# Kernel tuning notes

Hardware: AMD Instinct MI355X
Metric: run time of the kernel (lower is better)

## Reference

```python
import jax, jax.numpy as jnp
import numpy as np

DIM = 256
NUM_HEADS = 4
HEAD_DIM = DIM // NUM_HEADS


def setup_inputs() -> dict:
    key = jax.random.key(0)
    ks = jax.random.split(key, 8)
    B, N, C = 4, 2048, DIM
    x = jax.random.normal(ks[0], (B, N, C), dtype=jnp.float32)
    R = jax.random.normal(ks[1], (B, 3, 3), dtype=jnp.float32)
    P = jax.random.normal(ks[2], (N, 3), dtype=jnp.float32)
    s = 1.0 / np.sqrt(C)
    qkv_w = jax.random.normal(ks[3], (3 * C, C), dtype=jnp.float32) * s
    qkv_b = jax.random.normal(ks[4], (3 * C,), dtype=jnp.float32) * 0.02
    proj_w = jax.random.normal(ks[5], (C, C), dtype=jnp.float32) * s
    proj_b = jax.random.normal(ks[6], (C,), dtype=jnp.float32) * 0.02
    pos_scale = jnp.asarray(1.0, dtype=jnp.float32)
    return {"x": x, "R": R, "P": P, "qkv_w": qkv_w, "qkv_b": qkv_b,
            "proj_w": proj_w, "proj_b": proj_b, "pos_scale": pos_scale}


def reference(x, R, P, qkv_w, qkv_b, proj_w, proj_b, pos_scale):
    B, N, C = x.shape
    H, D = NUM_HEADS, HEAD_DIM
    scale = D ** -0.5
    # qkv: (B,N,3C) -> (3,B,H,N,D)
    qkv = (x @ qkv_w.T + qkv_b).reshape(B, N, 3, H, D).transpose(2, 0, 3, 1, 4)
    q, k, v = qkv[0], qkv[1], qkv[2]
    # attention logits (B,H,N,N)
    attn = jnp.einsum('bhid,bhjd->bhij', q, k) * scale
    # positional bias: RP = (R @ P^T)^T -> (B,N,3); bias_ij = dot(RP_i, P_j)
    RP = jnp.einsum('bab,jb->bja', R, P) if False else jnp.einsum('bca,ja->bjc', jnp.swapaxes(R, 1, 2), P)
    RP = jnp.einsum('bcd,jd->bjc', R, P)  # (B,N,3): (R @ P.T).T
    bias = jnp.einsum('bik,jk->bij', RP, P)[:, None, :, :] * pos_scale  # (B,1,N,N) broadcast over heads
    attn = jax.nn.softmax(attn + bias, axis=-1)
    out = jnp.einsum('bhij,bhjd->bhid', attn, v)  # (B,H,N,D)
    out = out.transpose(0, 2, 1, 3).reshape(B, N, C)
    out = out @ proj_w.T + proj_b
    return out
```

## Files before the change

kernel.cpp:

```cpp
#include <hip/hip_runtime.h>
#include <hip/hip_bf16.h>

#define B_ 4
#define N_ 2048
#define C_ 256
#define H_ 4
#define D_ 64

typedef __attribute__((ext_vector_type(8))) short bf16x8;
typedef __attribute__((ext_vector_type(4))) float f32x4;

#define LOG2E 1.4426950408889634f

static __device__ inline unsigned short f2bf(float f) {
    unsigned u = __builtin_bit_cast(unsigned, f);
    unsigned r = (u + 0x7fffu + ((u >> 16) & 1u)) >> 16;
    return (unsigned short)r;
}
static __device__ inline float bf2f(unsigned short h) {
    unsigned u = ((unsigned)h) << 16;
    return __builtin_bit_cast(float, u);
}
static __device__ inline unsigned pack2(float a, float b) {
    __hip_bfloat162 h = __float22bfloat162_rn(make_float2(a, b));
    unsigned u;
    __builtin_memcpy(&u, &h, 4);
    return u;
}
static __device__ inline bf16x8 ld_frag(const unsigned short* p) {
    return __builtin_bit_cast(bf16x8, *(const uint4*)p);
}

__global__ __launch_bounds__(256) void cvt_kernel(
    const float* __restrict__ x, const float* __restrict__ qkv_w,
    const float* __restrict__ proj_w,
    unsigned short* __restrict__ xb, unsigned short* __restrict__ wqb,
    unsigned short* __restrict__ wpb)
{
    const int bid = blockIdx.x, tid = threadIdx.x;
    const float* s; unsigned short* d; int i;
    if (bid < 1024)      { s = x;      d = xb;  i = (bid * 256 + tid) * 8; }
    else if (bid < 1120) { s = qkv_w;  d = wqb; i = ((bid - 1024) * 256 + tid) * 8; }
    else                 { s = proj_w; d = wpb; i = ((bid - 1120) * 256 + tid) * 8; }
    float4 a = *(const float4*)(s + i);
    float4 b = *(const float4*)(s + i + 4);
    uint4 u;
    u.x = pack2(a.x, a.y); u.y = pack2(a.z, a.w);
    u.z = pack2(b.x, b.y); u.w = pack2(b.z, b.w);
    *(uint4*)(d + i) = u;
}

__global__ __launch_bounds__(256) void qkv_gemm(
    const unsigned short* __restrict__ xb, const unsigned short* __restrict__ wb,
    const float* __restrict__ bias, unsigned short* __restrict__ qb,
    unsigned short* __restrict__ kb, unsigned short* __restrict__ vt)
{
    __shared__ __align__(16) unsigned short As[128 * 40];
    __shared__ __align__(16) unsigned short Bs[128 * 40];
    const int m0 = blockIdx.x * 128, o0 = blockIdx.y * 128;
    const int tid = threadIdx.x;
    const int wave = tid >> 6, lane = tid & 63, quad = lane >> 4, l16 = lane & 15;
    const int wy = wave >> 1, wx = wave & 1;

    f32x4 acc[4][4];
    #pragma unroll
    for (int i = 0; i < 4; ++i)
        #pragma unroll
        for (int j = 0; j < 4; ++j) acc[i][j] = (f32x4){0.f, 0.f, 0.f, 0.f};

    const int srow = tid >> 1, soff = (tid & 1) * 16;

    for (int k0 = 0; k0 < 256; k0 += 32) {
        __syncthreads();
        {
            const unsigned short* sa = &xb[(size_t)(m0 + srow) * 256 + k0 + soff];
            const unsigned short* sb = &wb[(size_t)(o0 + srow) * 256 + k0 + soff];
            *(uint4*)&As[srow * 40 + soff + 0] = *(const uint4*)(sa + 0);
            *(uint4*)&As[srow * 40 + soff + 8] = *(const uint4*)(sa + 8);
            *(uint4*)&Bs[srow * 40 + soff + 0] = *(const uint4*)(sb + 0);
            *(uint4*)&Bs[srow * 40 + soff + 8] = *(const uint4*)(sb + 8);
        }
        __syncthreads();
        bf16x8 a[4], b[4];
        #pragma unroll
        for (int mt = 0; mt < 4; ++mt) a[mt] = ld_frag(&As[(wy * 64 + mt * 16 + l16) * 40 + quad * 8]);
        #pragma unroll
        for (int nt = 0; nt < 4; ++nt) b[nt] = ld_frag(&Bs[(wx * 64 + nt * 16 + l16) * 40 + quad * 8]);
        #pragma unroll
        for (int mt = 0; mt < 4; ++mt)
            #pragma unroll
            for (int nt = 0; nt < 4; ++nt)
                acc[mt][nt] = __builtin_amdgcn_mfma_f32_16x16x32_bf16(a[mt], b[nt], acc[mt][nt], 0, 0, 0);
    }

    const int sec = o0 + wx * 64;
    const int three = sec >> 8;
    const int h = (sec >> 6) & 3;
    const int b = m0 >> 11;
    float bv[4];
    #pragma unroll
    for (int nt = 0; nt < 4; ++nt) bv[nt] = bias[sec + nt * 16 + l16];

    if (three == 2) {
        const int n64 = (m0 + wy * 64) & 2047;
        const size_t bh64 = ((size_t)b * H_ + h) * 64;
        #pragma unroll
        for (int nt = 0; nt < 4; ++nt) {
            int d = nt * 16 + l16;
            #pragma unroll
            for (int r = 0; r < 4; ++r) {
                ushort4 v;
                v.x = f2bf(acc[0][nt][r] + bv[nt]);
                v.y = f2bf(acc[1][nt][r] + bv[nt]);
                v.z = f2bf(acc[2][nt][r] + bv[nt]);
                v.w = f2bf(acc[3][nt][r] + bv[nt]);
                *(ushort4*)&vt[(bh64 + d) * N_ + n64 + 16 * quad + 4 * r] = v;
            }
        }
    } else {
        unsigned short* dst = (three == 0) ? qb : kb;
        float sc = (three == 0) ? (0.125f * LOG2E) : 1.0f;
        #pragma unroll
        for (int mt = 0; mt < 4; ++mt)
            #pragma unroll
            for (int r = 0; r < 4; ++r) {
                int n = (m0 + wy * 64 + mt * 16 + quad * 4 + r) & 2047;
                size_t rowbase = (((size_t)b * H_ + h) * N_ + n) * D_;
                #pragma unroll
                for (int nt = 0; nt < 4; ++nt)
                    dst[rowbase + nt * 16 + l16] = f2bf((acc[mt][nt][r] + bv[nt]) * sc);
            }
    }
}

#define LDK 72
#define LDKX 104

__global__ __launch_bounds__(256) void attn_kernel(
    const unsigned short* __restrict__ qb, const unsigned short* __restrict__ kb,
    const unsigned short* __restrict__ vt,
    const float* __restrict__ Rm, const float* __restrict__ Pm,
    const float* __restrict__ ps_ptr,
    unsigned short* __restrict__ Opart, float* __restrict__ ml)
{
    __shared__ __align__(16) unsigned short Ks[64 * LDKX];
    __shared__ __align__(16) unsigned short Vs[64 * LDK];
    __shared__ __align__(16) unsigned short Ps[64 * LDK];

    const int bh = blockIdx.y;
    const int b = bh >> 2;
    const int i0 = blockIdx.x * 64;
    const int split = blockIdx.z;
    const int tid = threadIdx.x;
    const int wave = tid >> 6, lane = tid & 63;
    const int quad = lane >> 4, l16 = lane & 15;
    const float ps = ps_ptr[0];

    const size_t base = (size_t)bh * N_ * D_;
    const unsigned short* qg = qb + base;
    const unsigned short* kg = kb + base;
    const unsigned short* vg = vt + base;

    if (tid < 64) {
        uint4 z = {0u, 0u, 0u, 0u};
        *(uint4*)&Ks[tid * LDKX + 80] = z;
        *(uint4*)&Ks[tid * LDKX + 88] = z;
    }

    const int qrow = i0 + wave * 16 + l16;
    bf16x8 aq[3];
    #pragma unroll
    for (int ks = 0; ks < 2; ++ks)
        aq[ks] = ld_frag(&qg[(size_t)qrow * D_ + ks * 32 + quad * 8]);

    {
        float p0 = Pm[qrow * 3 + 0], p1 = Pm[qrow * 3 + 1], p2 = Pm[qrow * 3 + 2];
        float sc = ps * LOG2E;
        unsigned short ah[3], al[3];
        #pragma unroll
        for (int c = 0; c < 3; ++c) {
            float a = (Rm[b * 9 + c * 3 + 0] * p0 + Rm[b * 9 + c * 3 + 1] * p1
                     + Rm[b * 9 + c * 3 + 2] * p2) * sc;
            ah[c] = f2bf(a);
            al[c] = f2bf(a - bf2f(ah[c]));
        }
        bf16x8 e = (bf16x8){0,0,0,0,0,0,0,0};
        if (quad == 0) {
            e[0] = (short)ah[0]; e[1] = (short)ah[1]; e[2] = (short)ah[2];
            e[3] = (short)ah[0]; e[4] = (short)ah[1]; e[5] = (short)ah[2];
            e[6] = (short)al[0]; e[7] = (short)al[1];
        } else if (quad == 1) {
            e[0] = (short)al[2];
        }
        aq[2] = e;
    }

    const bf16x8 ones = (bf16x8){0x3F80,0x3F80,0x3F80,0x3F80,0x3F80,0x3F80,0x3F80,0x3F80};

    float m_run = -1e30f;
    f32x4 o_acc[4], lacc;
    #pragma unroll
    for (int t = 0; t < 4; ++t) o_acc[t] = (f32x4){0.f, 0.f, 0.f, 0.f};
    lacc = (f32x4){0.f, 0.f, 0.f, 0.f};

    const int jbeg = split * (N_ / 2);
    const int NT = (N_ / 2) / 64;

    for (int jt = 0; jt < NT; ++jt) {
        const int j0 = jbeg + jt * 64;
        __syncthreads();
        #pragma unroll
        for (int rr = 0; rr < 2; ++rr) {
            int c = tid + rr * 256;
            int row = c >> 3, off = (c & 7) * 8;
            *(uint4*)&Ks[row * LDKX + off] = *(const uint4*)&kg[(size_t)(j0 + row) * D_ + off];
            *(uint4*)&Vs[row * LDK + off] = *(const uint4*)&vg[(size_t)row * N_ + j0 + off];
        }
        if (tid < 64) {
            const float* pp = &Pm[(size_t)(j0 + tid) * 3];
            float p0 = pp[0], p1 = pp[1], p2 = pp[2];
            unsigned u0 = f2bf(p0), u1 = f2bf(p1), u2 = f2bf(p2);
            unsigned v0 = f2bf(p0 - bf2f((unsigned short)u0));
            unsigned v1 = f2bf(p1 - bf2f((unsigned short)u1));
            unsigned v2 = f2bf(p2 - bf2f((unsigned short)u2));
            uint4 lo, hi;
            lo.x = u0 | (u1 << 16); lo.y = u2 | (v0 << 16);
            lo.z = v1 | (v2 << 16); lo.w = u0 | (u1 << 16);
            hi.x = u2; hi.y = 0u; hi.z = 0u; hi.w = 0u;
            *(uint4*)&Ks[tid * LDKX + 64] = lo;
            *(uint4*)&Ks[tid * LDKX + 72] = hi;
        }
        __syncthreads();

        f32x4 s[4];
        #pragma unroll
        for (int t = 0; t < 4; ++t) {
            f32x4 c = {0.f, 0.f, 0.f, 0.f};
            #pragma unroll
            for (int ks = 0; ks < 3; ++ks) {
                bf16x8 bk = ld_frag(&Ks[(l16 + 16 * t) * LDKX + ks * 32 + quad * 8]);
                c = __builtin_amdgcn_mfma_f32_16x16x32_bf16(aq[ks], bk, c, 0, 0, 0);
            }
            s[t] = c;
        }

        float mx = m_run;
        #pragma unroll
        for (int t = 0; t < 4; ++t)
            #pragma unroll
            for (int r = 0; r < 4; ++r)
                mx = fmaxf(mx, s[t][r]);
        #pragma unroll
        for (int off = 1; off < 64; off <<= 1)
            mx = fmaxf(mx, __shfl_xor(mx, off));
        const float alpha = exp2f(m_run - mx);
        m_run = mx;

        #pragma unroll
        for (int r = 0; r < 4; ++r) {
            float p0 = exp2f(s[0][r] - mx), p1 = exp2f(s[1][r] - mx);
            float p2 = exp2f(s[2][r] - mx), p3 = exp2f(s[3][r] - mx);
            uint2 w;
            w.x = pack2(p0, p1);
            w.y = pack2(p2, p3);
            *(uint2*)&Ps[(wave * 16 + quad * 4 + r) * LDK + 4 * l16] = w;
        }

        if (alpha < 1.0f) {
            #pragma unroll
            for (int t = 0; t < 4; ++t)
                #pragma unroll
                for (int r = 0; r < 4; ++r)
                    o_acc[t][r] *= alpha;
            #pragma unroll
            for (int r = 0; r < 4; ++r) lacc[r] *= alpha;
        }

        #pragma unroll
        for (int ks = 0; ks < 2; ++ks) {
            bf16x8 ap = ld_frag(&Ps[(wave * 16 + l16) * LDK + ks * 32 + quad * 8]);
            #pragma unroll
            for (int t = 0; t < 4; ++t) {
                bf16x8 bv = ld_frag(&Vs[(l16 + 16 * t) * LDK + ks * 32 + quad * 8]);
                o_acc[t] = __builtin_amdgcn_mfma_f32_16x16x32_bf16(ap, bv, o_acc[t], 0, 0, 0);
            }
            lacc = __builtin_amdgcn_mfma_f32_16x16x32_bf16(ap, ones, lacc, 0, 0, 0);
        }
    }

    const size_t pbase = (size_t)(split * 16 + bh) * N_;
    #pragma unroll
    for (int r = 0; r < 4; ++r) {
        int row = i0 + wave * 16 + quad * 4 + r;
        #pragma unroll
        for (int t = 0; t < 4; ++t)
            Opart[(pbase + row) * D_ + l16 + 16 * t] = f2bf(o_acc[t][r]);
        if (l16 == 0) {
            float2* mlp = (float2*)ml;
            mlp[pbase + row] = make_float2(m_run, lacc[r]);
        }
    }
}

__global__ __launch_bounds__(256) void proj_gemm(
    const unsigned short* __restrict__ Opart, const float* __restrict__ ml,
    const unsigned short* __restrict__ wb, const float* __restrict__ bias,
    float* __restrict__ out)
{
    __shared__ __align__(16) unsigned short As[64 * 40];
    __shared__ __align__(16) unsigned short Bs[64 * 40];
    const int m0 = blockIdx.x * 64, o0 = blockIdx.y * 64;
    const int tid = threadIdx.x;
    const int wave = tid >> 6, lane = tid & 63, quad = lane >> 4, l16 = lane & 15;
    const float2* mlp = (const float2*)ml;

    const int srow = tid >> 2, scb = (tid & 3) * 8;
    const int sm = m0 + srow, sb = sm >> 11, sn = sm & 2047;

    float w1h[4], w2h[4];
    #pragma unroll
    for (int h = 0; h < 4; ++h) {
        size_t r1 = (size_t)(sb * 4 + h) * N_ + sn;
        float2 ml1 = mlp[r1], ml2 = mlp[r1 + 16 * N_];
        float mm = fmaxf(ml1.x, ml2.x);
        float w1 = exp2f(ml1.x - mm), w2 = exp2f(ml2.x - mm);
        float inv = 1.f / (ml1.y * w1 + ml2.y * w2);
        w1h[h] = w1 * inv; w2h[h] = w2 * inv;
    }

    f32x4 acc[4];
    #pragma unroll
    for (int j = 0; j < 4; ++j) acc[j] = (f32x4){0.f, 0.f, 0.f, 0.f};

    for (int k0 = 0; k0 < 256; k0 += 32) {
        const int h = k0 >> 6;
        const int d0 = (k0 & 63) + scb;
        __syncthreads();
        {
            size_t r1 = (size_t)(sb * 4 + h) * N_ + sn;
            union { uint4 u; unsigned short s[8]; } a1, a2;
            a1.u = *(const uint4*)&Opart[r1 * D_ + d0];
            a2.u = *(const uint4*)&Opart[(r1 + 16 * N_) * D_ + d0];
            float w1 = w1h[h], w2 = w2h[h];
            uint4 mv;
            unsigned* mp = (unsigned*)&mv;
            #pragma unroll
            for (int j = 0; j < 4; ++j)
                mp[j] = pack2(bf2f(a1.s[2*j]) * w1 + bf2f(a2.s[2*j]) * w2,
                              bf2f(a1.s[2*j+1]) * w1 + bf2f(a2.s[2*j+1]) * w2);
            *(uint4*)&As[srow * 40 + scb] = mv;
            *(uint4*)&Bs[srow * 40 + scb] = *(const uint4*)&wb[(size_t)(o0 + srow) * 256 + k0 + scb];
        }
        __syncthreads();
        bf16x8 a = ld_frag(&As[(wave * 16 + l16) * 40 + quad * 8]);
        #pragma unroll
        for (int nt = 0; nt < 4; ++nt) {
            bf16x8 b = ld_frag(&Bs[(nt * 16 + l16) * 40 + quad * 8]);
            acc[nt] = __builtin_amdgcn_mfma_f32_16x16x32_bf16(a, b, acc[nt], 0, 0, 0);
        }
    }

    float bv[4];
    #pragma unroll
    for (int nt = 0; nt < 4; ++nt) bv[nt] = bias[o0 + nt * 16 + l16];
    #pragma unroll
    for (int r = 0; r < 4; ++r) {
        int m = m0 + wave * 16 + quad * 4 + r;
        #pragma unroll
        for (int nt = 0; nt < 4; ++nt)
            out[(size_t)m * 256 + o0 + nt * 16 + l16] = acc[nt][r] + bv[nt];
    }
}

extern "C" void kernel_launch(void* const* d_in, const int* in_sizes, int n_in,
                              void* d_out, int out_size, void* d_ws, size_t ws_size,
                              hipStream_t stream) {
    const float* x       = (const float*)d_in[0];
    const float* Rm      = (const float*)d_in[1];
    const float* Pm      = (const float*)d_in[2];
    const float* qkv_w   = (const float*)d_in[3];
    const float* qkv_b   = (const float*)d_in[4];
    const float* proj_w  = (const float*)d_in[5];
    const float* proj_b  = (const float*)d_in[6];
    const float* pos_scl = (const float*)d_in[7];
    float* out = (float*)d_out;

    const size_t NE = (size_t)B_ * H_ * N_ * D_;
    unsigned short* xb    = (unsigned short*)d_ws;
    unsigned short* wqb   = xb   + NE;
    unsigned short* wpb   = wqb  + 768 * 256;
    unsigned short* qb    = wpb  + 256 * 256;
    unsigned short* kb    = qb   + NE;
    unsigned short* vtb   = kb   + NE;
    unsigned short* opart = vtb  + NE;
    float*          mlb   = (float*)(opart + 2 * NE);

    cvt_kernel<<<1152, 256, 0, stream>>>(x, qkv_w, proj_w, xb, wqb, wpb);
    qkv_gemm<<<dim3(64, 6), 256, 0, stream>>>(xb, wqb, qkv_b, qb, kb, vtb);
    attn_kernel<<<dim3(32, 16, 2), 256, 0, stream>>>(qb, kb, vtb, Rm, Pm, pos_scl, opart, mlb);
    proj_gemm<<<dim3(128, 4), 256, 0, stream>>>(opart, mlb, wpb, proj_b, out);
}
```

Before: 140.1 us.

## Fuse all stages into one persistent kernel with grid-wide atomic barriers

```diff
diff --git a/kernel.cpp b/kernel.cpp
--- a/kernel.cpp
+++ b/kernel.cpp
@@ -6,6 +6,7 @@
 #define C_ 256
 #define H_ 4
 #define D_ 64
+#define GRID_ 512
 
 typedef __attribute__((ext_vector_type(8))) short bf16x8;
 typedef __attribute__((ext_vector_type(4))) float f32x4;
@@ -31,344 +32,320 @@
     return __builtin_bit_cast(bf16x8, *(const uint4*)p);
 }
 
-__global__ __launch_bounds__(256) void cvt_kernel(
-    const float* __restrict__ x, const float* __restrict__ qkv_w,
-    const float* __restrict__ proj_w,
-    unsigned short* __restrict__ xb, unsigned short* __restrict__ wqb,
-    unsigned short* __restrict__ wpb)
-{
-    const int bid = blockIdx.x, tid = threadIdx.x;
-    const float* s; unsigned short* d; int i;
-    if (bid < 1024)      { s = x;      d = xb;  i = (bid * 256 + tid) * 8; }
-    else if (bid < 1120) { s = qkv_w;  d = wqb; i = ((bid - 1024) * 256 + tid) * 8; }
-    else                 { s = proj_w; d = wpb; i = ((bid - 1120) * 256 + tid) * 8; }
-    float4 a = *(const float4*)(s + i);
-    float4 b = *(const float4*)(s + i + 4);
-    uint4 u;
-    u.x = pack2(a.x, a.y); u.y = pack2(a.z, a.w);
-    u.z = pack2(b.x, b.y); u.w = pack2(b.z, b.w);
-    *(uint4*)(d + i) = u;
-}
-
-__global__ __launch_bounds__(256) void qkv_gemm(
-    const unsigned short* __restrict__ xb, const unsigned short* __restrict__ wb,
-    const float* __restrict__ bias, unsigned short* __restrict__ qb,
-    unsigned short* __restrict__ kb, unsigned short* __restrict__ vt)
-{
-    __shared__ __align__(16) unsigned short As[128 * 40];
-    __shared__ __align__(16) unsigned short Bs[128 * 40];
-    const int m0 = blockIdx.x * 128, o0 = blockIdx.y * 128;
-    const int tid = threadIdx.x;
-    const int wave = tid >> 6, lane = tid & 63, quad = lane >> 4, l16 = lane & 15;
-    const int wy = wave >> 1, wx = wave & 1;
-
-    f32x4 acc[4][4];
-    #pragma unroll
-    for (int i = 0; i < 4; ++i)
-        #pragma unroll
-        for (int j = 0; j < 4; ++j) acc[i][j] = (f32x4){0.f, 0.f, 0.f, 0.f};
-
-    const int srow = tid >> 1, soff = (tid & 1) * 16;
-
-    for (int k0 = 0; k0 < 256; k0 += 32) {
-        __syncthreads();
-        {
-            const unsigned short* sa = &xb[(size_t)(m0 + srow) * 256 + k0 + soff];
-            const unsigned short* sb = &wb[(size_t)(o0 + srow) * 256 + k0 + soff];
-            *(uint4*)&As[srow * 40 + soff + 0] = *(const uint4*)(sa + 0);
-            *(uint4*)&As[srow * 40 + soff + 8] = *(const uint4*)(sa + 8);
-            *(uint4*)&Bs[srow * 40 + soff + 0] = *(const uint4*)(sb + 0);
-            *(uint4*)&Bs[srow * 40 + soff + 8] = *(const uint4*)(sb + 8);
-        }
-        __syncthreads();
-        bf16x8 a[4], b[4];
-        #pragma unroll
-        for (int mt = 0; mt < 4; ++mt) a[mt] = ld_frag(&As[(wy * 64 + mt * 16 + l16) * 40 + quad * 8]);
-        #pragma unroll
-        for (int nt = 0; nt < 4; ++nt) b[nt] = ld_frag(&Bs[(wx * 64 + nt * 16 + l16) * 40 + quad * 8]);
-        #pragma unroll
-        for (int mt = 0; mt < 4; ++mt)
-            #pragma unroll
-            for (int nt = 0; nt < 4; ++nt)
-                acc[mt][nt] = __builtin_amdgcn_mfma_f32_16x16x32_bf16(a[mt], b[nt], acc[mt][nt], 0, 0, 0);
-    }
-
-    const int sec = o0 + wx * 64;
-    const int three = sec >> 8;
-    const int h = (sec >> 6) & 3;
-    const int b = m0 >> 11;
-    float bv[4];
-    #pragma unroll
-    for (int nt = 0; nt < 4; ++nt) bv[nt] = bias[sec + nt * 16 + l16];
-
-    if (three == 2) {
-        const int n64 = (m0 + wy * 64) & 2047;
-        const size_t bh64 = ((size_t)b * H_ + h) * 64;
-        #pragma unroll
-        for (int nt = 0; nt < 4; ++nt) {
-            int d = nt * 16 + l16;
-            #pragma unroll
-            for (int r = 0; r < 4; ++r) {
-                ushort4 v;
-                v.x = f2bf(acc[0][nt][r] + bv[nt]);
-                v.y = f2bf(acc[1][nt][r] + bv[nt]);
-                v.z = f2bf(acc[2][nt][r] + bv[nt]);
-                v.w = f2bf(acc[3][nt][r] + bv[nt]);
-                *(ushort4*)&vt[(bh64 + d) * N_ + n64 + 16 * quad + 4 * r] = v;
-            }
-        }
-    } else {
-        unsigned short* dst = (three == 0) ? qb : kb;
-        float sc = (three == 0) ? (0.125f * LOG2E) : 1.0f;
-        #pragma unroll
-        for (int mt = 0; mt < 4; ++mt)
-            #pragma unroll
-            for (int r = 0; r < 4; ++r) {
-                int n = (m0 + wy * 64 + mt * 16 + quad * 4 + r) & 2047;
-                size_t rowbase = (((size_t)b * H_ + h) * N_ + n) * D_;
-                #pragma unroll
-                for (int nt = 0; nt < 4; ++nt)
-                    dst[rowbase + nt * 16 + l16] = f2bf((acc[mt][nt][r] + bv[nt]) * sc);
-            }
-    }
+static __device__ inline void gbar(unsigned* cnt, unsigned target) {
+    __syncthreads();
+    if (threadIdx.x == 0) {
+        __threadfence();
+        atomicAdd(cnt, 1u);
+        while (atomicAdd(cnt, 0u) < target)
+            __builtin_amdgcn_s_sleep(8);
+        __threadfence();
+    }
+    __syncthreads();
+}
+
+__global__ void init_kernel(unsigned* cnt) {
+    if (threadIdx.x < 4) cnt[threadIdx.x] = 0u;
 }
 
 #define LDK 72
 #define LDKX 104
 
-__global__ __launch_bounds__(256) void attn_kernel(
-    const unsigned short* __restrict__ qb, const unsigned short* __restrict__ kb,
-    const unsigned short* __restrict__ vt,
-    const float* __restrict__ Rm, const float* __restrict__ Pm,
-    const float* __restrict__ ps_ptr,
-    unsigned short* __restrict__ Opart, float* __restrict__ ml)
+__global__ __launch_bounds__(256) void fused_kernel(
+    const float* __restrict__ x, const float* __restrict__ Rm,
+    const float* __restrict__ Pm, const float* __restrict__ qkv_w,
+    const float* __restrict__ qkv_b, const float* __restrict__ proj_w,
+    const float* __restrict__ proj_b, const float* __restrict__ ps_ptr,
+    float* __restrict__ out,
+    unsigned short* __restrict__ xb, unsigned short* __restrict__ wqb,
+    unsigned short* __restrict__ wpb, unsigned short* __restrict__ qb,
+    unsigned short* __restrict__ kb, unsigned short* __restrict__ vt,
+    unsigned short* __restrict__ obuf, unsigned* __restrict__ cnt)
 {
-    __shared__ __align__(16) unsigned short Ks[64 * LDKX];
-    __shared__ __align__(16) unsigned short Vs[64 * LDK];
-    __shared__ __align__(16) unsigned short Ps[64 * LDK];
-
-    const int bh = blockIdx.y;
-    const int b = bh >> 2;
-    const int i0 = blockIdx.x * 64;
-    const int split = blockIdx.z;
+    __shared__ __align__(16) unsigned short smem[15872];
+
+    const int bid = blockIdx.x;
     const int tid = threadIdx.x;
     const int wave = tid >> 6, lane = tid & 63;
     const int quad = lane >> 4, l16 = lane & 15;
-    const float ps = ps_ptr[0];
-
-    const size_t base = (size_t)bh * N_ * D_;
-    const unsigned short* qg = qb + base;
-    const unsigned short* kg = kb + base;
-    const unsigned short* vg = vt + base;
-
-    if (tid < 64) {
-        uint4 z = {0u, 0u, 0u, 0u};
-        *(uint4*)&Ks[tid * LDKX + 80] = z;
-        *(uint4*)&Ks[tid * LDKX + 88] = z;
-    }
-
-    const int qrow = i0 + wave * 16 + l16;
-    bf16x8 aq[3];
-    #pragma unroll
-    for (int ks = 0; ks < 2; ++ks)
-        aq[ks] = ld_frag(&qg[(size_t)qrow * D_ + ks * 32 + quad * 8]);
 
     {
-        float p0 = Pm[qrow * 3 + 0], p1 = Pm[qrow * 3 + 1], p2 = Pm[qrow * 3 + 2];
-        float sc = ps * LOG2E;
-        unsigned short ah[3], al[3];
-        #pragma unroll
-        for (int c = 0; c < 3; ++c) {
-            float a = (Rm[b * 9 + c * 3 + 0] * p0 + Rm[b * 9 + c * 3 + 1] * p1
-                     + Rm[b * 9 + c * 3 + 2] * p2) * sc;
-            ah[c] = f2bf(a);
-            al[c] = f2bf(a - bf2f(ah[c]));
-        }
-        bf16x8 e = (bf16x8){0,0,0,0,0,0,0,0};
-        if (quad == 0) {
-            e[0] = (short)ah[0]; e[1] = (short)ah[1]; e[2] = (short)ah[2];
-            e[3] = (short)ah[0]; e[4] = (short)ah[1]; e[5] = (short)ah[2];
-            e[6] = (short)al[0]; e[7] = (short)al[1];
-        } else if (quad == 1) {
-            e[0] = (short)al[2];
-        }
-        aq[2] = e;
-    }
-
-    const bf16x8 ones = (bf16x8){0x3F80,0x3F80,0x3F80,0x3F80,0x3F80,0x3F80,0x3F80,0x3F80};
-
-    float m_run = -1e30f;
-    f32x4 o_acc[4], lacc;
-    #pragma unroll
-    for (int t = 0; t < 4; ++t) o_acc[t] = (f32x4){0.f, 0.f, 0.f, 0.f};
-    lacc = (f32x4){0.f, 0.f, 0.f, 0.f};
-
-    const int jbeg = split * (N_ / 2);
-    const int NT = (N_ / 2) / 64;
-
-    for (int jt = 0; jt < NT; ++jt) {
-        const int j0 = jbeg + jt * 64;
-        __syncthreads();
-        #pragma unroll
-        for (int rr = 0; rr < 2; ++rr) {
-            int c = tid + rr * 256;
-            int row = c >> 3, off = (c & 7) * 8;
-            *(uint4*)&Ks[row * LDKX + off] = *(const uint4*)&kg[(size_t)(j0 + row) * D_ + off];
-            *(uint4*)&Vs[row * LDK + off] = *(const uint4*)&vg[(size_t)row * N_ + j0 + off];
-        }
+        const int total8 = (2097152 + 196608 + 65536) / 8;
+        for (int i = bid * 256 + tid; i < total8; i += GRID_ * 256) {
+            int e = i * 8;
+            const float* s; unsigned short* d; int off;
+            if (e < 2097152)      { s = x;      d = xb;  off = e; }
+            else if (e < 2293760) { s = qkv_w;  d = wqb; off = e - 2097152; }
+            else                  { s = proj_w; d = wpb; off = e - 2293760; }
+            float4 a = *(const float4*)(s + off);
+            float4 b = *(const float4*)(s + off + 4);
+            uint4 u;
+            u.x = pack2(a.x, a.y); u.y = pack2(a.z, a.w);
+            u.z = pack2(b.x, b.y); u.w = pack2(b.z, b.w);
+            *(uint4*)(d + off) = u;
+        }
+    }
+    gbar(&cnt[0], GRID_);
+
+    if (bid < 384) {
+        unsigned short* As = smem;
+        unsigned short* Bs = smem + 5120;
+        const int m0 = (bid & 63) * 128, o0 = (bid >> 6) * 128;
+        const int wy = wave >> 1, wx = wave & 1;
+
+        f32x4 acc[4][4];
+        #pragma unroll
+        for (int i = 0; i < 4; ++i)
+            #pragma unroll
+            for (int j = 0; j < 4; ++j) acc[i][j] = (f32x4){0.f, 0.f, 0.f, 0.f};
+
+        const int srow = tid >> 1, soff = (tid & 1) * 16;
+
+        for (int k0 = 0; k0 < 256; k0 += 32) {
+            __syncthreads();
+            {
+                const unsigned short* sa = &xb[(size_t)(m0 + srow) * 256 + k0 + soff];
+                const unsigned short* sb = &wqb[(size_t)(o0 + srow) * 256 + k0 + soff];
+                *(uint4*)&As[srow * 40 + soff + 0] = *(const uint4*)(sa + 0);
+                *(uint4*)&As[srow * 40 + soff + 8] = *(const uint4*)(sa + 8);
+                *(uint4*)&Bs[srow * 40 + soff + 0] = *(const uint4*)(sb + 0);
+                *(uint4*)&Bs[srow * 40 + soff + 8] = *(const uint4*)(sb + 8);
+            }
+            __syncthreads();
+            bf16x8 a[4], b[4];
+            #pragma unroll
+            for (int mt = 0; mt < 4; ++mt) a[mt] = ld_frag(&As[(wy * 64 + mt * 16 + l16) * 40 + quad * 8]);
+            #pragma unroll
+            for (int nt = 0; nt < 4; ++nt) b[nt] = ld_frag(&Bs[(wx * 64 + nt * 16 + l16) * 40 + quad * 8]);
+            #pragma unroll
+            for (int mt = 0; mt < 4; ++mt)
+                #pragma unroll
+                for (int nt = 0; nt < 4; ++nt)
+                    acc[mt][nt] = __builtin_amdgcn_mfma_f32_16x16x32_bf16(a[mt], b[nt], acc[mt][nt], 0, 0, 0);
+        }
+
+        const int sec = o0 + wx * 64;
+        const int three = sec >> 8;
+        const int h = (sec >> 6) & 3;
+        const int b = m0 >> 11;
+        float bv[4];
+        #pragma unroll
+        for (int nt = 0; nt < 4; ++nt) bv[nt] = qkv_b[sec + nt * 16 + l16];
+
+        if (three == 2) {
+            const int n64 = (m0 + wy * 64) & 2047;
+            const size_t bh64 = ((size_t)b * H_ + h) * 64;
+            #pragma unroll
+            for (int nt = 0; nt < 4; ++nt) {
+                int d = nt * 16 + l16;
+                #pragma unroll
+                for (int r = 0; r < 4; ++r) {
+                    ushort4 v;
+                    v.x = f2bf(acc[0][nt][r] + bv[nt]);
+                    v.y = f2bf(acc[1][nt][r] + bv[nt]);
+                    v.z = f2bf(acc[2][nt][r] + bv[nt]);
+                    v.w = f2bf(acc[3][nt][r] + bv[nt]);
+                    *(ushort4*)&vt[(bh64 + d) * N_ + n64 + 16 * quad + 4 * r] = v;
+                }
+            }
+        } else {
+            unsigned short* dst = (three == 0) ? qb : kb;
+            float sc = (three == 0) ? (0.125f * LOG2E) : 1.0f;
+            #pragma unroll
+            for (int mt = 0; mt < 4; ++mt)
+                #pragma unroll
+                for (int r = 0; r < 4; ++r) {
+                    int n = (m0 + wy * 64 + mt * 16 + quad * 4 + r) & 2047;
+                    size_t rowbase = (((size_t)b * H_ + h) * N_ + n) * D_;
+                    #pragma unroll
+                    for (int nt = 0; nt < 4; ++nt)
+                        dst[rowbase + nt * 16 + l16] = f2bf((acc[mt][nt][r] + bv[nt]) * sc);
+                }
+        }
+    }
+    gbar(&cnt[1], GRID_);
+
+    {
+        unsigned short* Ks = smem;
+        unsigned short* Vs = smem + 6656;
+        unsigned short* Ps = smem + 11264;
+        const int i0 = (bid & 31) * 64;
+        const int bh = bid >> 5;
+        const int b = bh >> 2, h = bh & 3;
+        const float ps = ps_ptr[0];
+
+        const size_t base = (size_t)bh * N_ * D_;
+        const unsigned short* qg = qb + base;
+        const unsigned short* kg = kb + base;
+        const unsigned short* vg = vt + base;
+
         if (tid < 64) {
-            const float* pp = &Pm[(size_t)(j0 + tid) * 3];
-            float p0 = pp[0], p1 = pp[1], p2 = pp[2];
-            unsigned u0 = f2bf(p0), u1 = f2bf(p1), u2 = f2bf(p2);
-            unsigned v0 = f2bf(p0 - bf2f((unsigned short)u0));
-            unsigned v1 = f2bf(p1 - bf2f((unsigned short)u1));
-            unsigned v2 = f2bf(p2 - bf2f((unsigned short)u2));
-            uint4 lo, hi;
-            lo.x = u0 | (u1 << 16); lo.y = u2 | (v0 << 16);
-            lo.z = v1 | (v2 << 16); lo.w = u0 | (u1 << 16);
-            hi.x = u2; hi.y = 0u; hi.z = 0u; hi.w = 0u;
-            *(uint4*)&Ks[tid * LDKX + 64] = lo;
-            *(uint4*)&Ks[tid * LDKX + 72] = hi;
-        }
-        __syncthreads();
-
-        f32x4 s[4];
-        #pragma unroll
-        for (int t = 0; t < 4; ++t) {
-            f32x4 c = {0.f, 0.f, 0.f, 0.f};
-            #pragma unroll
-            for (int ks = 0; ks < 3; ++ks) {
-                bf16x8 bk = ld_frag(&Ks[(l16 + 16 * t) * LDKX + ks * 32 + quad * 8]);
-                c = __builtin_amdgcn_mfma_f32_16x16x32_bf16(aq[ks], bk, c, 0, 0, 0);
-            }
-            s[t] = c;
-        }
-
-        float mx = m_run;
-        #pragma unroll
-        for (int t = 0; t < 4; ++t)
-            #pragma unroll
-            for (int r = 0; r < 4; ++r)
-                mx = fmaxf(mx, s[t][r]);
-        #pragma unroll
-        for (int off = 1; off < 64; off <<= 1)
-            mx = fmaxf(mx, __shfl_xor(mx, off));
-        const float alpha = exp2f(m_run - mx);
-        m_run = mx;
+            uint4 z = {0u, 0u, 0u, 0u};
+            *(uint4*)&Ks[tid * LDKX + 80] = z;
+            *(uint4*)&Ks[tid * LDKX + 88] = z;
+        }
+
+        const int qrow = i0 + wave * 16 + l16;
+        bf16x8 aq[3];
+        #pragma unroll
+        for (int ks = 0; ks < 2; ++ks)
+            aq[ks] = ld_frag(&qg[(size_t)qrow * D_ + ks * 32 + quad * 8]);
+        {
+            float p0 = Pm[qrow * 3 + 0], p1 = Pm[qrow * 3 + 1], p2 = Pm[qrow * 3 + 2];
+            float sc = ps * LOG2E;
+            unsigned short ah[3], al[3];
+            #pragma unroll
+            for (int c = 0; c < 3; ++c) {
+                float a = (Rm[b * 9 + c * 3 + 0] * p0 + Rm[b * 9 + c * 3 + 1] * p1
+                         + Rm[b * 9 + c * 3 + 2] * p2) * sc;
+                ah[c] = f2bf(a);
+                al[c] = f2bf(a - bf2f(ah[c]));
+            }
+            bf16x8 e = (bf16x8){0,0,0,0,0,0,0,0};
+            if (quad == 0) {
+                e[0] = (short)ah[0]; e[1] = (short)ah[1]; e[2] = (short)ah[2];
+                e[3] = (short)ah[0]; e[4] = (short)ah[1]; e[5] = (short)ah[2];
+                e[6] = (short)al[0]; e[7] = (short)al[1];
+            } else if (quad == 1) {
+                e[0] = (short)al[2];
+            }
+            aq[2] = e;
+        }
+
+        const bf16x8 ones = (bf16x8){0x3F80,0x3F80,0x3F80,0x3F80,0x3F80,0x3F80,0x3F80,0x3F80};
+
+        float m_run = -1e30f;
+        f32x4 o_acc[4], lacc;
+        #pragma unroll
+        for (int t = 0; t < 4; ++t) o_acc[t] = (f32x4){0.f, 0.f, 0.f, 0.f};
+        lacc = (f32x4){0.f, 0.f, 0.f, 0.f};
+
+        for (int jt = 0; jt < N_ / 64; ++jt) {
+            const int j0 = jt * 64;
+            __syncthreads();
+            #pragma unroll
+            for (int rr = 0; rr < 2; ++rr) {
+                int c = tid + rr * 256;
+                int row = c >> 3, off = (c & 7) * 8;
+                *(uint4*)&Ks[row * LDKX + off] = *(const uint4*)&kg[(size_t)(j0 + row) * D_ + off];
+                *(uint4*)&Vs[row * LDK + off] = *(const uint4*)&vg[(size_t)row * N_ + j0 + off];
+            }
+            if (tid < 64) {
+                const float* pp = &Pm[(size_t)(j0 + tid) * 3];
+                float p0 = pp[0], p1 = pp[1], p2 = pp[2];
+                unsigned u0 = f2bf(p0), u1 = f2bf(p1), u2 = f2bf(p2);
+                unsigned v0 = f2bf(p0 - bf2f((unsigned short)u0));
+                unsigned v1 = f2bf(p1 - bf2f((unsigned short)u1));
+                unsigned v2 = f2bf(p2 - bf2f((unsigned short)u2));
+                uint4 lo, hi;
+                lo.x = u0 | (u1 << 16); lo.y = u2 | (v0 << 16);
+                lo.z = v1 | (v2 << 16); lo.w = u0 | (u1 << 16);
+                hi.x = u2; hi.y = 0u; hi.z = 0u; hi.w = 0u;
+                *(uint4*)&Ks[tid * LDKX + 64] = lo;
+                *(uint4*)&Ks[tid * LDKX + 72] = hi;
+            }
+            __syncthreads();
+
+            f32x4 s[4];
+            #pragma unroll
+            for (int t = 0; t < 4; ++t) {
+                f32x4 c = {0.f, 0.f, 0.f, 0.f};
+                #pragma unroll
+                for (int ks = 0; ks < 3; ++ks) {
+                    bf16x8 bk = ld_frag(&Ks[(l16 + 16 * t) * LDKX + ks * 32 + quad * 8]);
+                    c = __builtin_amdgcn_mfma_f32_16x16x32_bf16(aq[ks], bk, c, 0, 0, 0);
+                }
+                s[t] = c;
+            }
+
+            float mx = m_run;
+            #pragma unroll
+            for (int t = 0; t < 4; ++t)
+                #pragma unroll
+                for (int r = 0; r < 4; ++r)
+                    mx = fmaxf(mx, s[t][r]);
+            #pragma unroll
+            for (int off = 1; off < 64; off <<= 1)
+                mx = fmaxf(mx, __shfl_xor(mx, off));
+            const float alpha = exp2f(m_run - mx);
+            m_run = mx;
+
+            #pragma unroll
+            for (int r = 0; r < 4; ++r) {
+                float p0 = exp2f(s[0][r] - mx), p1 = exp2f(s[1][r] - mx);
+                float p2 = exp2f(s[2][r] - mx), p3 = exp2f(s[3][r] - mx);
+                uint2 w;
+                w.x = pack2(p0, p1);
+                w.y = pack2(p2, p3);
+                *(uint2*)&Ps[(wave * 16 + quad * 4 + r) * LDK + 4 * l16] = w;
+            }
+
+            if (alpha < 1.0f) {
+                #pragma unroll
+                for (int t = 0; t < 4; ++t)
+                    #pragma unroll
+                    for (int r = 0; r < 4; ++r)
+                        o_acc[t][r] *= alpha;
+                #pragma unroll
+                for (int r = 0; r < 4; ++r) lacc[r] *= alpha;
+            }
+
+            #pragma unroll
+            for (int ks = 0; ks < 2; ++ks) {
+                bf16x8 ap = ld_frag(&Ps[(wave * 16 + l16) * LDK + ks * 32 + quad * 8]);
+                #pragma unroll
+                for (int t = 0; t < 4; ++t) {
+                    bf16x8 bv = ld_frag(&Vs[(l16 + 16 * t) * LDK + ks * 32 + quad * 8]);
+                    o_acc[t] = __builtin_amdgcn_mfma_f32_16x16x32_bf16(ap, bv, o_acc[t], 0, 0, 0);
+                }
+                lacc = __builtin_amdgcn_mfma_f32_16x16x32_bf16(ap, ones, lacc, 0, 0, 0);
+            }
+        }
 
         #pragma unroll
         for (int r = 0; r < 4; ++r) {
-            float p0 = exp2f(s[0][r] - mx), p1 = exp2f(s[1][r] - mx);
-            float p2 = exp2f(s[2][r] - mx), p3 = exp2f(s[3][r] - mx);
-            uint2 w;
-            w.x = pack2(p0, p1);
-            w.y = pack2(p2, p3);
-            *(uint2*)&Ps[(wave * 16 + quad * 4 + r) * LDK + 4 * l16] = w;
-        }
-
-        if (alpha < 1.0f) {
+            float inv = 1.f / lacc[r];
+            int row = i0 + wave * 16 + quad * 4 + r;
             #pragma unroll
             for (int t = 0; t < 4; ++t)
-                #pragma unroll
-                for (int r = 0; r < 4; ++r)
-                    o_acc[t][r] *= alpha;
-            #pragma unroll
-            for (int r = 0; r < 4; ++r) lacc[r] *= alpha;
-        }
-
-        #pragma unroll
-        for (int ks = 0; ks < 2; ++ks) {
-            bf16x8 ap = ld_frag(&Ps[(wave * 16 + l16) * LDK + ks * 32 + quad * 8]);
-            #pragma unroll
-            for (int t = 0; t < 4; ++t) {
-                bf16x8 bv = ld_frag(&Vs[(l16 + 16 * t) * LDK + ks * 32 + quad * 8]);
-                o_acc[t] = __builtin_amdgcn_mfma_f32_16x16x32_bf16(ap, bv, o_acc[t], 0, 0, 0);
-            }
-            lacc = __builtin_amdgcn_mfma_f32_16x16x32_bf16(ap, ones, lacc, 0, 0, 0);
-        }
-    }
-
-    const size_t pbase = (size_t)(split * 16 + bh) * N_;
-    #pragma unroll
-    for (int r = 0; r < 4; ++r) {
-        int row = i0 + wave * 16 + quad * 4 + r;
-        #pragma unroll
-        for (int t = 0; t < 4; ++t)
-            Opart[(pbase + row) * D_ + l16 + 16 * t] = f2bf(o_acc[t][r]);
-        if (l16 == 0) {
-            float2* mlp = (float2*)ml;
-            mlp[pbase + row] = make_float2(m_run, lacc[r]);
-        }
-    }
-}
-
-__global__ __launch_bounds__(256) void proj_gemm(
-    const unsigned short* __restrict__ Opart, const float* __restrict__ ml,
-    const unsigned short* __restrict__ wb, const float* __restrict__ bias,
-    float* __restrict__ out)
-{
-    __shared__ __align__(16) unsigned short As[64 * 40];
-    __shared__ __align__(16) unsigned short Bs[64 * 40];
-    const int m0 = blockIdx.x * 64, o0 = blockIdx.y * 64;
-    const int tid = threadIdx.x;
-    const int wave = tid >> 6, lane = tid & 63, quad = lane >> 4, l16 = lane & 15;
-    const float2* mlp = (const float2*)ml;
-
-    const int srow = tid >> 2, scb = (tid & 3) * 8;
-    const int sm = m0 + srow, sb = sm >> 11, sn = sm & 2047;
-
-    float w1h[4], w2h[4];
-    #pragma unroll
-    for (int h = 0; h < 4; ++h) {
-        size_t r1 = (size_t)(sb * 4 + h) * N_ + sn;
-        float2 ml1 = mlp[r1], ml2 = mlp[r1 + 16 * N_];
-        float mm = fmaxf(ml1.x, ml2.x);
-        float w1 = exp2f(ml1.x - mm), w2 = exp2f(ml2.x - mm);
-        float inv = 1.f / (ml1.y * w1 + ml2.y * w2);
-        w1h[h] = w1 * inv; w2h[h] = w2 * inv;
-    }
-
-    f32x4 acc[4];
-    #pragma unroll
-    for (int j = 0; j < 4; ++j) acc[j] = (f32x4){0.f, 0.f, 0.f, 0.f};
-
-    for (int k0 = 0; k0 < 256; k0 += 32) {
-        const int h = k0 >> 6;
-        const int d0 = (k0 & 63) + scb;
-        __syncthreads();
-        {
-            size_t r1 = (size_t)(sb * 4 + h) * N_ + sn;
-            union { uint4 u; unsigned short s[8]; } a1, a2;
-            a1.u = *(const uint4*)&Opart[r1 * D_ + d0];
-            a2.u = *(const uint4*)&Opart[(r1 + 16 * N_) * D_ + d0];
-            float w1 = w1h[h], w2 = w2h[h];
-            uint4 mv;
-            unsigned* mp = (unsigned*)&mv;
-            #pragma unroll
-            for (int j = 0; j < 4; ++j)
-                mp[j] = pack2(bf2f(a1.s[2*j]) * w1 + bf2f(a2.s[2*j]) * w2,
-                              bf2f(a1.s[2*j+1]) * w1 + bf2f(a2.s[2*j+1]) * w2);
-            *(uint4*)&As[srow * 40 + scb] = mv;
-            *(uint4*)&Bs[srow * 40 + scb] = *(const uint4*)&wb[(size_t)(o0 + srow) * 256 + k0 + scb];
-        }
-        __syncthreads();
-        bf16x8 a = ld_frag(&As[(wave * 16 + l16) * 40 + quad * 8]);
-        #pragma unroll
-        for (int nt = 0; nt < 4; ++nt) {
-            bf16x8 b = ld_frag(&Bs[(nt * 16 + l16) * 40 + quad * 8]);
-            acc[nt] = __builtin_amdgcn_mfma_f32_16x16x32_bf16(a, b, acc[nt], 0, 0, 0);
-        }
-    }
-
-    float bv[4];
-    #pragma unroll
-    for (int nt = 0; nt < 4; ++nt) bv[nt] = bias[o0 + nt * 16 + l16];
-    #pragma unroll
-    for (int r = 0; r < 4; ++r) {
-        int m = m0 + wave * 16 + quad * 4 + r;
-        #pragma unroll
-        for (int nt = 0; nt < 4; ++nt)
-            out[(size_t)m * 256 + o0 + nt * 16 + l16] = acc[nt][r] + bv[nt];
+                obuf[((size_t)b * N_ + row) * C_ + h * 64 + l16 + 16 * t] = f2bf(o_acc[t][r] * inv);
+        }
+    }
+    gbar(&cnt[2], GRID_);
+
+    {
+        unsigned short* As = smem;
+        unsigned short* Bs = smem + 2560;
+        const int m0 = (bid & 127) * 64, o0 = (bid >> 7) * 64;
+        const int srow = tid >> 2, scb = (tid & 3) * 8;
+
+        f32x4 acc[4];
+        #pragma unroll
+        for (int j = 0; j < 4; ++j) acc[j] = (f32x4){0.f, 0.f, 0.f, 0.f};
+
+        for (int k0 = 0; k0 < 256; k0 += 32) {
+            __syncthreads();
+            *(uint4*)&As[srow * 40 + scb] = *(const uint4*)&obuf[(size_t)(m0 + srow) * 256 + k0 + scb];
+            *(uint4*)&Bs[srow * 40 + scb] = *(const uint4*)&wpb[(size_t)(o0 + srow) * 256 + k0 + scb];
+            __syncthreads();
+            bf16x8 a = ld_frag(&As[(wave * 16 + l16) * 40 + quad * 8]);
+            #pragma unroll
+            for (int nt = 0; nt < 4; ++nt) {
+                bf16x8 b = ld_frag(&Bs[(nt * 16 + l16) * 40 + quad * 8]);
+                acc[nt] = __builtin_amdgcn_mfma_f32_16x16x32_bf16(a, b, acc[nt], 0, 0, 0);
+            }
+        }
+
+        float bv[4];
+        #pragma unroll
+        for (int nt = 0; nt < 4; ++nt) bv[nt] = proj_b[o0 + nt * 16 + l16];
+        #pragma unroll
+        for (int r = 0; r < 4; ++r) {
+            int m = m0 + wave * 16 + quad * 4 + r;
+            #pragma unroll
+            for (int nt = 0; nt < 4; ++nt)
+                out[(size_t)m * 256 + o0 + nt * 16 + l16] = acc[nt][r] + bv[nt];
+        }
     }
 }
 
@@ -386,17 +363,17 @@
     float* out = (float*)d_out;
 
     const size_t NE = (size_t)B_ * H_ * N_ * D_;
-    unsigned short* xb    = (unsigned short*)d_ws;
-    unsigned short* wqb   = xb   + NE;
-    unsigned short* wpb   = wqb  + 768 * 256;
-    unsigned short* qb    = wpb  + 256 * 256;
-    unsigned short* kb    = qb   + NE;
-    unsigned short* vtb   = kb   + NE;
-    unsigned short* opart = vtb  + NE;
-    float*          mlb   = (float*)(opart + 2 * NE);
-
-    cvt_kernel<<<1152, 256, 0, stream>>>(x, qkv_w, proj_w, xb, wqb, wpb);
-    qkv_gemm<<<dim3(64, 6), 256, 0, stream>>>(xb, wqb, qkv_b, qb, kb, vtb);
-    attn_kernel<<<dim3(32, 16, 2), 256, 0, stream>>>(qb, kb, vtb, Rm, Pm, pos_scl, opart, mlb);
-    proj_gemm<<<dim3(128, 4), 256, 0, stream>>>(opart, mlb, wpb, proj_b, out);
-}
+    unsigned short* xb   = (unsigned short*)d_ws;
+    unsigned short* wqb  = xb   + NE;
+    unsigned short* wpb  = wqb  + 768 * 256;
+    unsigned short* qb   = wpb  + 256 * 256;
+    unsigned short* kb   = qb   + NE;
+    unsigned short* vtb  = kb   + NE;
+    unsigned short* obuf = vtb  + NE;
+    unsigned* cnt = (unsigned*)(obuf + NE);
+
+    init_kernel<<<1, 64, 0, stream>>>(cnt);
+    fused_kernel<<<GRID_, 256, 0, stream>>>(x, Rm, Pm, qkv_w, qkv_b, proj_w, proj_b,
+                                            pos_scl, out, xb, wqb, wpb, qb, kb, vtb,
+                                            obuf, cnt);
+}
```

New measurement: 305.9 us. 118% more time.

## Process two query groups per attention block and split keys four ways

Applied to the files above, without the earlier changes.

```diff
diff --git a/kernel.cpp b/kernel.cpp
--- a/kernel.cpp
+++ b/kernel.cpp
@@ -149,7 +149,7 @@
 
     const int bh = blockIdx.y;
     const int b = bh >> 2;
-    const int i0 = blockIdx.x * 64;
+    const int i0 = blockIdx.x * 128;
     const int split = blockIdx.z;
     const int tid = threadIdx.x;
     const int wave = tid >> 6, lane = tid & 63;
@@ -161,19 +161,20 @@
     const unsigned short* kg = kb + base;
     const unsigned short* vg = vt + base;
 
-    if (tid < 64) {
+    if (quad == 1) {
+        int key = wave * 16 + l16;
         uint4 z = {0u, 0u, 0u, 0u};
-        *(uint4*)&Ks[tid * LDKX + 80] = z;
-        *(uint4*)&Ks[tid * LDKX + 88] = z;
-    }
-
-    const int qrow = i0 + wave * 16 + l16;
-    bf16x8 aq[3];
-    #pragma unroll
-    for (int ks = 0; ks < 2; ++ks)
-        aq[ks] = ld_frag(&qg[(size_t)qrow * D_ + ks * 32 + quad * 8]);
-
-    {
+        *(uint4*)&Ks[key * LDKX + 80] = z;
+        *(uint4*)&Ks[key * LDKX + 88] = z;
+    }
+
+    bf16x8 aq[2][3];
+    #pragma unroll
+    for (int g = 0; g < 2; ++g) {
+        const int qrow = i0 + g * 64 + wave * 16 + l16;
+        #pragma unroll
+        for (int ks = 0; ks < 2; ++ks)
+            aq[g][ks] = ld_frag(&qg[(size_t)qrow * D_ + ks * 32 + quad * 8]);
         float p0 = Pm[qrow * 3 + 0], p1 = Pm[qrow * 3 + 1], p2 = Pm[qrow * 3 + 2];
         float sc = ps * LOG2E;
         unsigned short ah[3], al[3];
@@ -192,19 +193,22 @@
         } else if (quad == 1) {
             e[0] = (short)al[2];
         }
-        aq[2] = e;
+        aq[g][2] = e;
     }
 
     const bf16x8 ones = (bf16x8){0x3F80,0x3F80,0x3F80,0x3F80,0x3F80,0x3F80,0x3F80,0x3F80};
 
-    float m_run = -1e30f;
-    f32x4 o_acc[4], lacc;
-    #pragma unroll
-    for (int t = 0; t < 4; ++t) o_acc[t] = (f32x4){0.f, 0.f, 0.f, 0.f};
-    lacc = (f32x4){0.f, 0.f, 0.f, 0.f};
-
-    const int jbeg = split * (N_ / 2);
-    const int NT = (N_ / 2) / 64;
+    float m_run[2] = {-1e30f, -1e30f};
+    f32x4 o_acc[2][4], lacc[2];
+    #pragma unroll
+    for (int g = 0; g < 2; ++g) {
+        #pragma unroll
+        for (int t = 0; t < 4; ++t) o_acc[g][t] = (f32x4){0.f, 0.f, 0.f, 0.f};
+        lacc[g] = (f32x4){0.f, 0.f, 0.f, 0.f};
+    }
+
+    const int jbeg = split * (N_ / 4);
+    const int NT = (N_ / 4) / 64;
 
     for (int jt = 0; jt < NT; ++jt) {
         const int j0 = jbeg + jt * 64;
@@ -216,8 +220,9 @@
             *(uint4*)&Ks[row * LDKX + off] = *(const uint4*)&kg[(size_t)(j0 + row) * D_ + off];
             *(uint4*)&Vs[row * LDK + off] = *(const uint4*)&vg[(size_t)row * N_ + j0 + off];
         }
-        if (tid < 64) {
-            const float* pp = &Pm[(size_t)(j0 + tid) * 3];
+        if (quad == 0) {
+            int key = wave * 16 + l16;
+            const float* pp = &Pm[(size_t)(j0 + key) * 3];
             float p0 = pp[0], p1 = pp[1], p2 = pp[2];
             unsigned u0 = f2bf(p0), u1 = f2bf(p1), u2 = f2bf(p2);
             unsigned v0 = f2bf(p0 - bf2f((unsigned short)u0));
@@ -227,79 +232,91 @@
             lo.x = u0 | (u1 << 16); lo.y = u2 | (v0 << 16);
             lo.z = v1 | (v2 << 16); lo.w = u0 | (u1 << 16);
             hi.x = u2; hi.y = 0u; hi.z = 0u; hi.w = 0u;
-            *(uint4*)&Ks[tid * LDKX + 64] = lo;
-            *(uint4*)&Ks[tid * LDKX + 72] = hi;
-        }
-        __syncthreads();
-
-        f32x4 s[4];
+            *(uint4*)&Ks[key * LDKX + 64] = lo;
+            *(uint4*)&Ks[key * LDKX + 72] = hi;
+        }
+        __syncthreads();
+
+        f32x4 s[2][4];
         #pragma unroll
         for (int t = 0; t < 4; ++t) {
-            f32x4 c = {0.f, 0.f, 0.f, 0.f};
-            #pragma unroll
-            for (int ks = 0; ks < 3; ++ks) {
-                bf16x8 bk = ld_frag(&Ks[(l16 + 16 * t) * LDKX + ks * 32 + quad * 8]);
-                c = __builtin_amdgcn_mfma_f32_16x16x32_bf16(aq[ks], bk, c, 0, 0, 0);
-            }
-            s[t] = c;
-        }
-
-        float mx = m_run;
-        #pragma unroll
-        for (int t = 0; t < 4; ++t)
-            #pragma unroll
-            for (int r = 0; r < 4; ++r)
-                mx = fmaxf(mx, s[t][r]);
-        #pragma unroll
-        for (int off = 1; off < 64; off <<= 1)
-            mx = fmaxf(mx, __shfl_xor(mx, off));
-        const float alpha = exp2f(m_run - mx);
-        m_run = mx;
-
-        #pragma unroll
-        for (int r = 0; r < 4; ++r) {
-            float p0 = exp2f(s[0][r] - mx), p1 = exp2f(s[1][r] - mx);
-            float p2 = exp2f(s[2][r] - mx), p3 = exp2f(s[3][r] - mx);
-            uint2 w;
-            w.x = pack2(p0, p1);
-            w.y = pack2(p2, p3);
-            *(uint2*)&Ps[(wave * 16 + quad * 4 + r) * LDK + 4 * l16] = w;
-        }
-
-        if (alpha < 1.0f) {
+            bf16x8 bk0 = ld_frag(&Ks[(l16 + 16 * t) * LDKX + 0 + quad * 8]);
+            bf16x8 bk1 = ld_frag(&Ks[(l16 + 16 * t) * LDKX + 32 + quad * 8]);
+            bf16x8 bk2 = ld_frag(&Ks[(l16 + 16 * t) * LDKX + 64 + quad * 8]);
+            #pragma unroll
+            for (int g = 0; g < 2; ++g) {
+                f32x4 c = {0.f, 0.f, 0.f, 0.f};
+                c = __builtin_amdgcn_mfma_f32_16x16x32_bf16(aq[g][0], bk0, c, 0, 0, 0);
+                c = __builtin_amdgcn_mfma_f32_16x16x32_bf16(aq[g][1], bk1, c, 0, 0, 0);
+                c = __builtin_amdgcn_mfma_f32_16x16x32_bf16(aq[g][2], bk2, c, 0, 0, 0);
+                s[g][t] = c;
+            }
+        }
+
+        float alpha[2];
+        #pragma unroll
+        for (int g = 0; g < 2; ++g) {
+            float mx = m_run[g];
             #pragma unroll
             for (int t = 0; t < 4; ++t)
                 #pragma unroll
                 for (int r = 0; r < 4; ++r)
-                    o_acc[t][r] *= alpha;
-            #pragma unroll
-            for (int r = 0; r < 4; ++r) lacc[r] *= alpha;
-        }
-
-        #pragma unroll
-        for (int ks = 0; ks < 2; ++ks) {
-            bf16x8 ap = ld_frag(&Ps[(wave * 16 + l16) * LDK + ks * 32 + quad * 8]);
-            #pragma unroll
-            for (int t = 0; t < 4; ++t) {
-                bf16x8 bv = ld_frag(&Vs[(l16 + 16 * t) * LDK + ks * 32 + quad * 8]);
-                o_acc[t] = __builtin_amdgcn_mfma_f32_16x16x32_bf16(ap, bv, o_acc[t], 0, 0, 0);
-            }
-            lacc = __builtin_amdgcn_mfma_f32_16x16x32_bf16(ap, ones, lacc, 0, 0, 0);
+                    mx = fmaxf(mx, s[g][t][r]);
+            #pragma unroll
+            for (int off = 1; off < 64; off <<= 1)
+                mx = fmaxf(mx, __shfl_xor(mx, off));
+            alpha[g] = exp2f(m_run[g] - mx);
+            m_run[g] = mx;
+        }
+
+        #pragma unroll
+        for (int g = 0; g < 2; ++g) {
+            const float mx = m_run[g];
+            #pragma unroll
+            for (int r = 0; r < 4; ++r) {
+                float p0 = exp2f(s[g][0][r] - mx), p1 = exp2f(s[g][1][r] - mx);
+                float p2 = exp2f(s[g][2][r] - mx), p3 = exp2f(s[g][3][r] - mx);
+                uint2 w;
+                w.x = pack2(p0, p1);
+                w.y = pack2(p2, p3);
+                *(uint2*)&Ps[(wave * 16 + quad * 4 + r) * LDK + 4 * l16] = w;
+            }
+            if (alpha[g] < 1.0f) {
+                #pragma unroll
+                for (int t = 0; t < 4; ++t)
+                    #pragma unroll
+                    for (int r = 0; r < 4; ++r)
+                        o_acc[g][t][r] *= alpha[g];
+                #pragma unroll
+                for (int r = 0; r < 4; ++r) lacc[g][r] *= alpha[g];
+            }
+            #pragma unroll
+            for (int ks = 0; ks < 2; ++ks) {
+                bf16x8 ap = ld_frag(&Ps[(wave * 16 + l16) * LDK + ks * 32 + quad * 8]);
+                #pragma unroll
+                for (int t = 0; t < 4; ++t) {
+                    bf16x8 bv = ld_frag(&Vs[(l16 + 16 * t) * LDK + ks * 32 + quad * 8]);
+                    o_acc[g][t] = __builtin_amdgcn_mfma_f32_16x16x32_bf16(ap, bv, o_acc[g][t], 0, 0, 0);
+                }
+                lacc[g] = __builtin_amdgcn_mfma_f32_16x16x32_bf16(ap, ones, lacc[g], 0, 0, 0);
+            }
         }
     }
 
     const size_t pbase = (size_t)(split * 16 + bh) * N_;
     #pragma unroll
-    for (int r = 0; r < 4; ++r) {
-        int row = i0 + wave * 16 + quad * 4 + r;
-        #pragma unroll
-        for (int t = 0; t < 4; ++t)
-            Opart[(pbase + row) * D_ + l16 + 16 * t] = f2bf(o_acc[t][r]);
-        if (l16 == 0) {
-            float2* mlp = (float2*)ml;
-            mlp[pbase + row] = make_float2(m_run, lacc[r]);
-        }
-    }
+    for (int g = 0; g < 2; ++g)
+        #pragma unroll
+        for (int r = 0; r < 4; ++r) {
+            int row = i0 + g * 64 + wave * 16 + quad * 4 + r;
+            #pragma unroll
+            for (int t = 0; t < 4; ++t)
+                Opart[(pbase + row) * D_ + l16 + 16 * t] = f2bf(o_acc[g][t][r]);
+            if (l16 == 0) {
+                float2* mlp = (float2*)ml;
+                mlp[pbase + row] = make_float2(m_run[g], lacc[g][r]);
+            }
+        }
 }
 
 __global__ __launch_bounds__(256) void proj_gemm(
@@ -317,15 +334,18 @@
     const int srow = tid >> 2, scb = (tid & 3) * 8;
     const int sm = m0 + srow, sb = sm >> 11, sn = sm & 2047;
 
-    float w1h[4], w2h[4];
+    float wgt[4][4];
     #pragma unroll
     for (int h = 0; h < 4; ++h) {
         size_t r1 = (size_t)(sb * 4 + h) * N_ + sn;
-        float2 ml1 = mlp[r1], ml2 = mlp[r1 + 16 * N_];
-        float mm = fmaxf(ml1.x, ml2.x);
-        float w1 = exp2f(ml1.x - mm), w2 = exp2f(ml2.x - mm);
-        float inv = 1.f / (ml1.y * w1 + ml2.y * w2);
-        w1h[h] = w1 * inv; w2h[h] = w2 * inv;
+        float2 m0v = mlp[r1], m1v = mlp[r1 + 16 * N_];
+        float2 m2v = mlp[r1 + 32 * N_], m3v = mlp[r1 + 48 * N_];
+        float mm = fmaxf(fmaxf(m0v.x, m1v.x), fmaxf(m2v.x, m3v.x));
+        float w0 = exp2f(m0v.x - mm), w1 = exp2f(m1v.x - mm);
+        float w2 = exp2f(m2v.x - mm), w3 = exp2f(m3v.x - mm);
+        float inv = 1.f / (m0v.y * w0 + m1v.y * w1 + m2v.y * w2 + m3v.y * w3);
+        wgt[h][0] = w0 * inv; wgt[h][1] = w1 * inv;
+        wgt[h][2] = w2 * inv; wgt[h][3] = w3 * inv;
     }
 
     f32x4 acc[4];
@@ -338,16 +358,22 @@
         __syncthreads();
         {
             size_t r1 = (size_t)(sb * 4 + h) * N_ + sn;
-            union { uint4 u; unsigned short s[8]; } a1, a2;
-            a1.u = *(const uint4*)&Opart[r1 * D_ + d0];
-            a2.u = *(const uint4*)&Opart[(r1 + 16 * N_) * D_ + d0];
-            float w1 = w1h[h], w2 = w2h[h];
+            union { uint4 u; unsigned short s[8]; } a0, a1, a2, a3;
+            a0.u = *(const uint4*)&Opart[r1 * D_ + d0];
+            a1.u = *(const uint4*)&Opart[(r1 + 16 * N_) * D_ + d0];
+            a2.u = *(const uint4*)&Opart[(r1 + 32 * N_) * D_ + d0];
+            a3.u = *(const uint4*)&Opart[(r1 + 48 * N_) * D_ + d0];
+            float w0 = wgt[h][0], w1 = wgt[h][1], w2 = wgt[h][2], w3 = wgt[h][3];
             uint4 mv;
             unsigned* mp = (unsigned*)&mv;
             #pragma unroll
-            for (int j = 0; j < 4; ++j)
-                mp[j] = pack2(bf2f(a1.s[2*j]) * w1 + bf2f(a2.s[2*j]) * w2,
-                              bf2f(a1.s[2*j+1]) * w1 + bf2f(a2.s[2*j+1]) * w2);
+            for (int j = 0; j < 4; ++j) {
+                float lo = bf2f(a0.s[2*j]) * w0 + bf2f(a1.s[2*j]) * w1
+                         + bf2f(a2.s[2*j]) * w2 + bf2f(a3.s[2*j]) * w3;
+                float hi = bf2f(a0.s[2*j+1]) * w0 + bf2f(a1.s[2*j+1]) * w1
+                         + bf2f(a2.s[2*j+1]) * w2 + bf2f(a3.s[2*j+1]) * w3;
+                mp[j] = pack2(lo, hi);
+            }
             *(uint4*)&As[srow * 40 + scb] = mv;
             *(uint4*)&Bs[srow * 40 + scb] = *(const uint4*)&wb[(size_t)(o0 + srow) * 256 + k0 + scb];
         }
@@ -393,10 +419,10 @@
     unsigned short* kb    = qb   + NE;
     unsigned short* vtb   = kb   + NE;
     unsigned short* opart = vtb  + NE;
-    float*          mlb   = (float*)(opart + 2 * NE);
+    float*          mlb   = (float*)(opart + 4 * NE);
 
     cvt_kernel<<<1152, 256, 0, stream>>>(x, qkv_w, proj_w, xb, wqb, wpb);
     qkv_gemm<<<dim3(64, 6), 256, 0, stream>>>(xb, wqb, qkv_b, qb, kb, vtb);
-    attn_kernel<<<dim3(32, 16, 2), 256, 0, stream>>>(qb, kb, vtb, Rm, Pm, pos_scl, opart, mlb);
+    attn_kernel<<<dim3(16, 16, 4), 256, 0, stream>>>(qb, kb, vtb, Rm, Pm, pos_scl, opart, mlb);
     proj_gemm<<<dim3(128, 4), 256, 0, stream>>>(opart, mlb, wpb, proj_b, out);
 }
```

Measured after the change: 151.1 us. 7.9% more time.
